# Kernel optimization log

Hardware: AMD Instinct MI355X
Metric: run time of the kernel (lower is better)

The kernel has to match this reference:

```python
import jax, jax.numpy as jnp
import numpy as np

B, V, NB, NJ, NEXTRA = 512, 6890, 10, 24, 9
PARENTS = np.array([-1,0,0,0,1,2,3,4,5,6,7,8,9,9,9,12,13,14,16,17,18,19,20,21], dtype=np.int32)


def setup_inputs() -> dict:
    key = jax.random.key(0)
    ks = jax.random.split(key, 11)
    betas = jax.random.normal(ks[0], (B, NB + 1), jnp.float32) * 0.1
    betas = betas.at[:, 0].set(1.0)  # col 0 is a global scale in this SMPL variant
    body_pose = jax.random.normal(ks[1], (B, 3 * (NJ - 1)), jnp.float32) * 0.2
    global_orient = jax.random.normal(ks[2], (B, 3), jnp.float32) * 0.2
    transl = jax.random.normal(ks[3], (B, 3), jnp.float32) * 0.1
    model_scale_opt = jnp.ones((1,), jnp.float32)
    smpl_v_template = jax.random.normal(ks[4], (V, 3), jnp.float32)
    smil_v_template = jax.random.normal(ks[5], (V, 3), jnp.float32)
    shapedirs = jax.random.normal(ks[6], (V, 3, NB), jnp.float32) * 0.01
    J_regressor = jax.nn.softmax(jax.random.normal(ks[7], (NJ, V), jnp.float32), axis=1)
    lbs_weights = jax.nn.softmax(jax.random.normal(ks[8], (V, NJ), jnp.float32) * 4.0, axis=1)
    J_regressor_extra = jax.nn.softmax(jax.random.normal(ks[9], (NEXTRA, V), jnp.float32), axis=1)
    parents = jnp.asarray(PARENTS)
    return dict(betas=betas, body_pose=body_pose, global_orient=global_orient,
                transl=transl, model_scale_opt=model_scale_opt,
                smpl_v_template=smpl_v_template, smil_v_template=smil_v_template,
                shapedirs=shapedirs, J_regressor=J_regressor, lbs_weights=lbs_weights,
                J_regressor_extra=J_regressor_extra, parents=parents)


def batch_rodrigues(rvecs):
    # rvecs: [N,3] axis-angle -> [N,3,3] rotation matrices
    angle = jnp.linalg.norm(rvecs + 1e-8, axis=1, keepdims=True)  # [N,1]
    axis = rvecs / angle
    c = jnp.cos(angle)[..., None]  # [N,1,1]
    s = jnp.sin(angle)[..., None]
    rx, ry, rz = axis[:, 0], axis[:, 1], axis[:, 2]
    z = jnp.zeros_like(rx)
    K = jnp.stack([z, -rz, ry, rz, z, -rx, -ry, rx, z], axis=1).reshape(-1, 3, 3)
    I = jnp.eye(3, dtype=rvecs.dtype)
    return I + s * K + (1.0 - c) * jnp.matmul(K, K)


def _smpl_forward(betas, body_pose, global_orient, transl, model_scale_opt,
                  smpl_v_template, smil_v_template, shapedirs,
                  J_regressor, lbs_weights, J_regressor_extra):
    dtype = betas.dtype
    # ---- updateShape ----
    s = model_scale_opt[0]
    v_template = smpl_v_template * s + (1.0 - s) * smil_v_template  # [V,3]
    blend_shape = jnp.einsum('bl,mkl->bmk', betas[:, 1:], shapedirs)  # [B,V,3]
    v_shaped = (v_template[None] + blend_shape) * betas[:, :1, None]  # scale col
    J_shaped = jnp.einsum('bik,ji->bjk', v_shaped, J_regressor)  # [B,NJ,3]

    # ---- updatePose ----
    full_pose = jnp.concatenate([global_orient, body_pose], axis=1)  # [B,NJ*3]
    rot_mats = batch_rodrigues(full_pose.reshape(-1, 3)).reshape(B, NJ, 3, 3)

    # relative joint locations w.r.t. parents
    rel_joints = J_shaped.at[:, 1:].add(-J_shaped[:, PARENTS[1:]])
    top = jnp.concatenate([rot_mats, rel_joints[..., None]], axis=-1)  # [B,NJ,3,4]
    bottom = jnp.broadcast_to(
        jnp.array([0.0, 0.0, 0.0, 1.0], dtype=dtype), (B, NJ, 1, 4))
    mats = jnp.concatenate([top, bottom], axis=2)  # [B,NJ,4,4]

    # sequential kinematic-chain composition over the 24-joint tree
    chain = [mats[:, 0]]
    for i in range(1, NJ):
        chain.append(jnp.matmul(chain[PARENTS[i]], mats[:, i]))
    chain = jnp.stack(chain, axis=1)  # [B,NJ,4,4]
    posed_joints = chain[:, :, :3, 3]  # [B,NJ,3]

    # relative transforms: subtract rotated rest joints
    corr = jnp.einsum('bjmn,bjn->bjm', chain[:, :, :3, :3], J_shaped)
    A = chain.at[:, :, :3, 3].add(-corr)  # [B,NJ,4,4]

    # linear blend skinning
    T = jnp.einsum('vj,bjmn->bvmn', lbs_weights, A)  # [B,V,4,4]
    verts = jnp.einsum('bvmn,bvn->bvm', T[:, :, :3, :3], v_shaped) + T[:, :, :3, 3]

    extra_joints = jnp.einsum('bik,ji->bjk', verts, J_regressor_extra)  # [B,9,3]
    joints = jnp.concatenate([posed_joints, extra_joints], axis=1)  # [B,33,3]

    t = transl[:, None, :]
    # concat verts and joints along point dim for a single output array
    return jnp.concatenate([verts + t, joints + t], axis=1)  # [B, V+33, 3]


def reference(betas, body_pose, global_orient, transl, model_scale_opt,
              smpl_v_template, smil_v_template, shapedirs,
              J_regressor, lbs_weights, J_regressor_extra, parents):
    return _smpl_forward(betas, body_pose, global_orient, transl, model_scale_opt,
                         smpl_v_template, smil_v_template, shapedirs,
                         J_regressor, lbs_weights, J_regressor_extra)
```

## Files before the change

kernel.cpp:

```cpp
#include <hip/hip_runtime.h>


#define BATCH 512
#define NV 6890
#define NBD 10
#define NJ 24
#define NEXTRA 9
#define NOUT (NV + NJ + NEXTRA)
#define VBLK ((NV + 255) / 256)
#define BPB 4
#define ECHUNK ((NV + 3) / 4)
#define PCHUNK 8
#define PCLEN ((NV + PCHUNK - 1) / PCHUNK)

__constant__ int c_par[NJ] = {-1,0,0,0,1,2,3,4,5,6,7,8,9,9,9,12,13,14,16,17,18,19,20,21};
__constant__ int c_dep[NJ] = {0,1,1,1,2,2,2,3,3,3,4,4,4,4,4,5,5,5,6,6,7,7,8,8};

__global__ __launch_bounds__(256) void precompute_kernel(
    const float* __restrict__ jreg,
    const float* __restrict__ smpl_t,
    const float* __restrict__ smil_t,
    const float* __restrict__ sdirs,
    const float* __restrict__ msc,
    float* __restrict__ jtjs_part)
{
    const int c = blockIdx.x;
    const int j = blockIdx.y;
    const float s = msc[0];

    const int vbeg = c * PCLEN;
    const int vend_ = (vbeg + PCLEN < NV) ? vbeg + PCLEN : NV;

    float acc[33];
#pragma unroll
    for (int i = 0; i < 33; ++i) acc[i] = 0.f;

    for (int v = vbeg + threadIdx.x; v < vend_; v += 256) {
        const float w = jreg[j * NV + v];
#pragma unroll
        for (int k = 0; k < 3; ++k) {
            float vt = s * smpl_t[v * 3 + k] + (1.f - s) * smil_t[v * 3 + k];
            acc[k] = fmaf(w, vt, acc[k]);
        }
        const float2* sd2 = (const float2*)(sdirs + (size_t)v * 30);
#pragma unroll
        for (int i = 0; i < 15; ++i) {
            float2 x = sd2[i];
            acc[3 + 2 * i]     = fmaf(w, x.x, acc[3 + 2 * i]);
            acc[3 + 2 * i + 1] = fmaf(w, x.y, acc[3 + 2 * i + 1]);
        }
    }

#pragma unroll
    for (int i = 0; i < 33; ++i) {
        float x = acc[i];
        for (int off = 32; off; off >>= 1) x += __shfl_xor(x, off, 64);
        acc[i] = x;
    }

    __shared__ float red[4][33];
    const int lane = threadIdx.x & 63, wv = threadIdx.x >> 6;
    if (lane == 0) {
#pragma unroll
        for (int i = 0; i < 33; ++i) red[wv][i] = acc[i];
    }
    __syncthreads();
    if (threadIdx.x < 33) {
        jtjs_part[(c * NJ + j) * 33 + threadIdx.x] =
            red[0][threadIdx.x] + red[1][threadIdx.x]
          + red[2][threadIdx.x] + red[3][threadIdx.x];
    }
}

__global__ __launch_bounds__(64) void joints_kernel(
    const float* __restrict__ betas,
    const float* __restrict__ body_pose,
    const float* __restrict__ glob_or,
    const float* __restrict__ transl,
    const float* __restrict__ jtjs_part,
    float* __restrict__ wsA,
    float* __restrict__ out)
{
    const int b = blockIdx.x;
    const int j = threadIdx.x;

    __shared__ float sJ[NJ][3];
    __shared__ float mats[NJ][12];
    __shared__ float chain[NJ][12];
    __shared__ float sbeta[NBD + 1];

    if (threadIdx.x < NBD + 1) sbeta[threadIdx.x] = betas[b * (NBD + 1) + threadIdx.x];

    if (threadIdx.x >= NJ && threadIdx.x < NJ + 3 * NEXTRA)
        out[((size_t)b * NOUT + NV + NJ) * 3 + (threadIdx.x - NJ)] = 0.f;

    __syncthreads();

    if (j < NJ) {
        float jt[33];
#pragma unroll
        for (int i = 0; i < 33; ++i) jt[i] = 0.f;
        for (int c = 0; c < PCHUNK; ++c) {
#pragma unroll
            for (int i = 0; i < 33; ++i) jt[i] += jtjs_part[(c * NJ + j) * 33 + i];
        }

        const float beta0 = sbeta[0];
#pragma unroll
        for (int k = 0; k < 3; ++k) {
            float a = jt[k];
#pragma unroll
            for (int l = 0; l < NBD; ++l) a = fmaf(sbeta[1 + l], jt[3 + k * 10 + l], a);
            sJ[j][k] = a * beta0;
        }
        float rx, ry, rz;
        if (j == 0) {
            rx = glob_or[b * 3 + 0]; ry = glob_or[b * 3 + 1]; rz = glob_or[b * 3 + 2];
        } else {
            rx = body_pose[b * 69 + (j - 1) * 3 + 0];
            ry = body_pose[b * 69 + (j - 1) * 3 + 1];
            rz = body_pose[b * 69 + (j - 1) * 3 + 2];
        }
        float ex = rx + 1e-8f, ey = ry + 1e-8f, ez = rz + 1e-8f;
        float ang = sqrtf(ex * ex + ey * ey + ez * ez);
        float inv = 1.f / ang;
        float ax = rx * inv, ay = ry * inv, az = rz * inv;
        float c = cosf(ang), s = sinf(ang), t = 1.f - c;
        mats[j][0]  = 1.f + t * (-(ay * ay + az * az));
        mats[j][1]  = -s * az + t * (ax * ay);
        mats[j][2]  =  s * ay + t * (ax * az);
        mats[j][4]  =  s * az + t * (ax * ay);
        mats[j][5]  = 1.f + t * (-(ax * ax + az * az));
        mats[j][6]  = -s * ax + t * (ay * az);
        mats[j][8]  = -s * ay + t * (ax * az);
        mats[j][9]  =  s * ax + t * (ay * az);
        mats[j][10] = 1.f + t * (-(ax * ax + ay * ay));
    }
    __syncthreads();
    if (j < NJ) {
        const int p = c_par[j];
        float t0 = sJ[j][0], t1 = sJ[j][1], t2 = sJ[j][2];
        if (p >= 0) { t0 -= sJ[p][0]; t1 -= sJ[p][1]; t2 -= sJ[p][2]; }
        mats[j][3] = t0; mats[j][7] = t1; mats[j][11] = t2;
    }
    __syncthreads();
    if (j == 0) {
#pragma unroll
        for (int k = 0; k < 12; ++k) chain[0][k] = mats[0][k];
    }
    __syncthreads();
    for (int lev = 1; lev <= 8; ++lev) {
        if (j < NJ && c_dep[j] == lev) {
            const int p = c_par[j];
            float r_[12];
#pragma unroll
            for (int r = 0; r < 3; ++r) {
#pragma unroll
                for (int col = 0; col < 4; ++col) {
                    float acc = (col == 3) ? chain[p][r * 4 + 3] : 0.f;
#pragma unroll
                    for (int q = 0; q < 3; ++q) acc = fmaf(chain[p][r * 4 + q], mats[j][q * 4 + col], acc);
                    r_[r * 4 + col] = acc;
                }
            }
#pragma unroll
            for (int k = 0; k < 12; ++k) chain[j][k] = r_[k];
        }
        __syncthreads();
    }
    if (j < NJ) {
        float A[12];
#pragma unroll
        for (int k = 0; k < 12; ++k) A[k] = chain[j][k];
        const float c0 = A[3], c1 = A[7], c2 = A[11];
        const float j0 = sJ[j][0], j1 = sJ[j][1], j2 = sJ[j][2];
        A[3]  = c0 - (A[0] * j0 + A[1] * j1 + A[2]  * j2);
        A[7]  = c1 - (A[4] * j0 + A[5] * j1 + A[6]  * j2);
        A[11] = c2 - (A[8] * j0 + A[9] * j1 + A[10] * j2);
#pragma unroll
        for (int k = 0; k < 12; ++k) wsA[((size_t)b * NJ + j) * 12 + k] = A[k];
        const float tx = transl[b * 3 + 0], ty = transl[b * 3 + 1], tz = transl[b * 3 + 2];
        const size_t o = ((size_t)b * NOUT + NV + j) * 3;
        out[o + 0] = c0 + tx; out[o + 1] = c1 + ty; out[o + 2] = c2 + tz;
    }
}

__global__ __launch_bounds__(256) void lbs_kernel(
    const float* __restrict__ betas,
    const float* __restrict__ transl,
    const float* __restrict__ msc,
    const float* __restrict__ smpl_t,
    const float* __restrict__ smil_t,
    const float* __restrict__ sdirs,
    const float* __restrict__ lbsw,
    const float* __restrict__ wsA,
    float* __restrict__ out)
{
    const int v = blockIdx.x * 256 + threadIdx.x;
    const bool valid = v < NV;
    const int vc = valid ? v : NV - 1;
    const int b0 = blockIdx.y * BPB;
    const float s = msc[0];

    float vt[3];
#pragma unroll
    for (int k = 0; k < 3; ++k)
        vt[k] = s * smpl_t[vc * 3 + k] + (1.f - s) * smil_t[vc * 3 + k];

    float sd[30];
    {
        const float2* sd2 = (const float2*)(sdirs + (size_t)vc * 30);
#pragma unroll
        for (int i = 0; i < 15; ++i) { float2 x = sd2[i]; sd[2 * i] = x.x; sd[2 * i + 1] = x.y; }
    }
    float w[NJ];
    {
        const float4* w4 = (const float4*)(lbsw + (size_t)vc * NJ);
#pragma unroll
        for (int i = 0; i < 6; ++i) {
            float4 x = w4[i];
            w[4 * i] = x.x; w[4 * i + 1] = x.y; w[4 * i + 2] = x.z; w[4 * i + 3] = x.w;
        }
    }

#pragma unroll
    for (int bb = 0; bb < BPB; ++bb) {
        const int b = b0 + bb;
        const float* __restrict__ Bb = betas + b * (NBD + 1);
        const float* __restrict__ Ab = wsA + (size_t)b * NJ * 12;

        float vs[3];
#pragma unroll
        for (int k = 0; k < 3; ++k) {
            float a = vt[k];
#pragma unroll
            for (int l = 0; l < NBD; ++l) a = fmaf(Bb[1 + l], sd[k * 10 + l], a);
            vs[k] = a * Bb[0];
        }

        float T[12];
#pragma unroll
        for (int k = 0; k < 12; ++k) T[k] = 0.f;
#pragma unroll 4
        for (int jj = 0; jj < NJ; ++jj) {
            const float ww = w[jj];
#pragma unroll
            for (int k = 0; k < 12; ++k) T[k] = fmaf(ww, Ab[jj * 12 + k], T[k]);
        }

        if (valid) {
            const float tx = transl[b * 3 + 0], ty = transl[b * 3 + 1], tz = transl[b * 3 + 2];
            const size_t o = ((size_t)b * NOUT + v) * 3;
            out[o + 0] = fmaf(T[0], vs[0], fmaf(T[1], vs[1], fmaf(T[2],  vs[2], T[3])))  + tx;
            out[o + 1] = fmaf(T[4], vs[0], fmaf(T[5], vs[1], fmaf(T[6],  vs[2], T[7])))  + ty;
            out[o + 2] = fmaf(T[8], vs[0], fmaf(T[9], vs[1], fmaf(T[10], vs[2], T[11]))) + tz;
        }
    }
}

__global__ __launch_bounds__(256) void extra_kernel(
    const float* __restrict__ jre,
    float* out)
{
    const int b = blockIdx.y;
    const int v0 = blockIdx.x * ECHUNK;
    int vend = v0 + ECHUNK; if (vend > NV) vend = NV;
    const float* vb = out + (size_t)b * NOUT * 3;

    float acc[27];
#pragma unroll
    for (int i = 0; i < 27; ++i) acc[i] = 0.f;

    for (int v = v0 + threadIdx.x; v < vend; v += 256) {
        const float x = vb[v * 3 + 0], y = vb[v * 3 + 1], z = vb[v * 3 + 2];
#pragma unroll
        for (int e = 0; e < NEXTRA; ++e) {
            const float we = jre[e * NV + v];
            acc[e * 3 + 0] = fmaf(we, x, acc[e * 3 + 0]);
            acc[e * 3 + 1] = fmaf(we, y, acc[e * 3 + 1]);
            acc[e * 3 + 2] = fmaf(we, z, acc[e * 3 + 2]);
        }
    }

#pragma unroll
    for (int i = 0; i < 27; ++i) {
        float x = acc[i];
        for (int off = 32; off; off >>= 1) x += __shfl_xor(x, off, 64);
        acc[i] = x;
    }
    __shared__ float red[4][27];
    const int lane = threadIdx.x & 63, wv = threadIdx.x >> 6;
    if (lane == 0) {
#pragma unroll
        for (int i = 0; i < 27; ++i) red[wv][i] = acc[i];
    }
    __syncthreads();
    if (threadIdx.x < 27) {
        const float sum = red[0][threadIdx.x] + red[1][threadIdx.x]
                        + red[2][threadIdx.x] + red[3][threadIdx.x];
        atomicAdd(&out[((size_t)b * NOUT + NV + NJ) * 3 + threadIdx.x], sum);
    }
}

extern "C" void kernel_launch(void* const* d_in, const int* in_sizes, int n_in,
                              void* d_out, int out_size, void* d_ws, size_t ws_size,
                              hipStream_t stream) {
    const float* betas     = (const float*)d_in[0];
    const float* body_pose = (const float*)d_in[1];
    const float* glob_or   = (const float*)d_in[2];
    const float* transl    = (const float*)d_in[3];
    const float* msc       = (const float*)d_in[4];
    const float* smpl_t    = (const float*)d_in[5];
    const float* smil_t    = (const float*)d_in[6];
    const float* sdirs     = (const float*)d_in[7];
    const float* jreg      = (const float*)d_in[8];
    const float* lbsw      = (const float*)d_in[9];
    const float* jre       = (const float*)d_in[10];

    float* out  = (float*)d_out;
    float* ws   = (float*)d_ws;
    float* wsA       = ws;
    float* jtjs_part = ws + (size_t)BATCH * NJ * 12;

    dim3 gA(PCHUNK, NJ);
    precompute_kernel<<<gA, 256, 0, stream>>>(jreg, smpl_t, smil_t, sdirs, msc, jtjs_part);

    joints_kernel<<<BATCH, 64, 0, stream>>>(betas, body_pose, glob_or, transl, jtjs_part, wsA, out);

    dim3 gC(VBLK, BATCH / BPB);
    lbs_kernel<<<gC, 256, 0, stream>>>(betas, transl, msc, smpl_t, smil_t, sdirs, lbsw, wsA, out);

    dim3 gE(4, BATCH);
    extra_kernel<<<gE, 256, 0, stream>>>(jre, out);
}
```

Measured before the change: 175.3 us.

## Compute extra joints algebraically from joint transforms instead of re-reading posed vertices

Because extra joints are linear in the per-joint transforms, the change precomputes, for each extra joint and body joint, the regressor-times-skinning-weight contractions of the template and shape directions, which do not depend on the batch. The joints kernel then forms the extra joints from these precomputed sums, the betas and the 24 transforms. This removes the extra_kernel pass, which re-read all posed vertices for every batch element and used atomics. The cost is extra blocks in the precompute kernel, and the floating-point summation order changes.

```diff
diff --git a/kernel.cpp b/kernel.cpp
--- a/kernel.cpp
+++ b/kernel.cpp
@@ -9,66 +9,111 @@
 #define NOUT (NV + NJ + NEXTRA)
 #define VBLK ((NV + 255) / 256)
 #define BPB 4
-#define ECHUNK ((NV + 3) / 4)
 #define PCHUNK 8
 #define PCLEN ((NV + PCHUNK - 1) / PCHUNK)
+#define EPN 34
 
 __constant__ int c_par[NJ] = {-1,0,0,0,1,2,3,4,5,6,7,8,9,9,9,12,13,14,16,17,18,19,20,21};
 __constant__ int c_dep[NJ] = {0,1,1,1,2,2,2,3,3,3,4,4,4,4,4,5,5,5,6,6,7,7,8,8};
 
-__global__ __launch_bounds__(256) void precompute_kernel(
+__global__ __launch_bounds__(256) void pre_kernel(
     const float* __restrict__ jreg,
+    const float* __restrict__ jre,
+    const float* __restrict__ lbsw,
     const float* __restrict__ smpl_t,
     const float* __restrict__ smil_t,
     const float* __restrict__ sdirs,
     const float* __restrict__ msc,
-    float* __restrict__ jtjs_part)
+    float* __restrict__ jtjs_part,
+    float* __restrict__ epre)
 {
-    const int c = blockIdx.x;
     const int j = blockIdx.y;
     const float s = msc[0];
 
-    const int vbeg = c * PCLEN;
-    const int vend_ = (vbeg + PCLEN < NV) ? vbeg + PCLEN : NV;
-
-    float acc[33];
-#pragma unroll
-    for (int i = 0; i < 33; ++i) acc[i] = 0.f;
-
-    for (int v = vbeg + threadIdx.x; v < vend_; v += 256) {
-        const float w = jreg[j * NV + v];
-#pragma unroll
-        for (int k = 0; k < 3; ++k) {
-            float vt = s * smpl_t[v * 3 + k] + (1.f - s) * smil_t[v * 3 + k];
-            acc[k] = fmaf(w, vt, acc[k]);
-        }
-        const float2* sd2 = (const float2*)(sdirs + (size_t)v * 30);
-#pragma unroll
-        for (int i = 0; i < 15; ++i) {
-            float2 x = sd2[i];
-            acc[3 + 2 * i]     = fmaf(w, x.x, acc[3 + 2 * i]);
-            acc[3 + 2 * i + 1] = fmaf(w, x.y, acc[3 + 2 * i + 1]);
-        }
-    }
-
-#pragma unroll
-    for (int i = 0; i < 33; ++i) {
-        float x = acc[i];
-        for (int off = 32; off; off >>= 1) x += __shfl_xor(x, off, 64);
-        acc[i] = x;
-    }
-
-    __shared__ float red[4][33];
+    __shared__ float red[4][EPN];
     const int lane = threadIdx.x & 63, wv = threadIdx.x >> 6;
-    if (lane == 0) {
-#pragma unroll
-        for (int i = 0; i < 33; ++i) red[wv][i] = acc[i];
-    }
-    __syncthreads();
-    if (threadIdx.x < 33) {
-        jtjs_part[(c * NJ + j) * 33 + threadIdx.x] =
-            red[0][threadIdx.x] + red[1][threadIdx.x]
-          + red[2][threadIdx.x] + red[3][threadIdx.x];
+
+    if (blockIdx.x < PCHUNK) {
+        const int c = blockIdx.x;
+        const int vbeg = c * PCLEN;
+        const int vend_ = (vbeg + PCLEN < NV) ? vbeg + PCLEN : NV;
+
+        float acc[33];
+#pragma unroll
+        for (int i = 0; i < 33; ++i) acc[i] = 0.f;
+
+        for (int v = vbeg + threadIdx.x; v < vend_; v += 256) {
+            const float w = jreg[j * NV + v];
+#pragma unroll
+            for (int k = 0; k < 3; ++k) {
+                float vt = s * smpl_t[v * 3 + k] + (1.f - s) * smil_t[v * 3 + k];
+                acc[k] = fmaf(w, vt, acc[k]);
+            }
+            const float2* sd2 = (const float2*)(sdirs + (size_t)v * 30);
+#pragma unroll
+            for (int i = 0; i < 15; ++i) {
+                float2 x = sd2[i];
+                acc[3 + 2 * i]     = fmaf(w, x.x, acc[3 + 2 * i]);
+                acc[3 + 2 * i + 1] = fmaf(w, x.y, acc[3 + 2 * i + 1]);
+            }
+        }
+
+#pragma unroll
+        for (int i = 0; i < 33; ++i) {
+            float x = acc[i];
+            for (int off = 32; off; off >>= 1) x += __shfl_xor(x, off, 64);
+            acc[i] = x;
+        }
+        if (lane == 0) {
+#pragma unroll
+            for (int i = 0; i < 33; ++i) red[wv][i] = acc[i];
+        }
+        __syncthreads();
+        if (threadIdx.x < 33) {
+            jtjs_part[(c * NJ + j) * 33 + threadIdx.x] =
+                red[0][threadIdx.x] + red[1][threadIdx.x]
+              + red[2][threadIdx.x] + red[3][threadIdx.x];
+        }
+    } else {
+        const int e = blockIdx.x - PCHUNK;
+
+        float acc[EPN];
+#pragma unroll
+        for (int i = 0; i < EPN; ++i) acc[i] = 0.f;
+
+        for (int v = threadIdx.x; v < NV; v += 256) {
+            const float u = jre[e * NV + v] * lbsw[(size_t)v * NJ + j];
+            acc[33] += u;
+#pragma unroll
+            for (int k = 0; k < 3; ++k) {
+                float vt = s * smpl_t[v * 3 + k] + (1.f - s) * smil_t[v * 3 + k];
+                acc[k] = fmaf(u, vt, acc[k]);
+            }
+            const float2* sd2 = (const float2*)(sdirs + (size_t)v * 30);
+#pragma unroll
+            for (int i = 0; i < 15; ++i) {
+                float2 x = sd2[i];
+                acc[3 + 2 * i]     = fmaf(u, x.x, acc[3 + 2 * i]);
+                acc[3 + 2 * i + 1] = fmaf(u, x.y, acc[3 + 2 * i + 1]);
+            }
+        }
+
+#pragma unroll
+        for (int i = 0; i < EPN; ++i) {
+            float x = acc[i];
+            for (int off = 32; off; off >>= 1) x += __shfl_xor(x, off, 64);
+            acc[i] = x;
+        }
+        if (lane == 0) {
+#pragma unroll
+            for (int i = 0; i < EPN; ++i) red[wv][i] = acc[i];
+        }
+        __syncthreads();
+        if (threadIdx.x < EPN) {
+            epre[(e * NJ + j) * EPN + threadIdx.x] =
+                red[0][threadIdx.x] + red[1][threadIdx.x]
+              + red[2][threadIdx.x] + red[3][threadIdx.x];
+        }
     }
 }
 
@@ -78,6 +123,7 @@
     const float* __restrict__ glob_or,
     const float* __restrict__ transl,
     const float* __restrict__ jtjs_part,
+    const float* __restrict__ epre,
     float* __restrict__ wsA,
     float* __restrict__ out)
 {
@@ -88,12 +134,10 @@
     __shared__ float mats[NJ][12];
     __shared__ float chain[NJ][12];
     __shared__ float sbeta[NBD + 1];
+    __shared__ float sS[NEXTRA][NJ][3];
+    __shared__ float sW[NEXTRA][NJ];
 
     if (threadIdx.x < NBD + 1) sbeta[threadIdx.x] = betas[b * (NBD + 1) + threadIdx.x];
-
-    if (threadIdx.x >= NJ && threadIdx.x < NJ + 3 * NEXTRA)
-        out[((size_t)b * NOUT + NV + NJ) * 3 + (threadIdx.x - NJ)] = 0.f;
-
     __syncthreads();
 
     if (j < NJ) {
@@ -179,9 +223,42 @@
         A[11] = c2 - (A[8] * j0 + A[9] * j1 + A[10] * j2);
 #pragma unroll
         for (int k = 0; k < 12; ++k) wsA[((size_t)b * NJ + j) * 12 + k] = A[k];
+#pragma unroll
+        for (int k = 0; k < 12; ++k) mats[j][k] = A[k];
         const float tx = transl[b * 3 + 0], ty = transl[b * 3 + 1], tz = transl[b * 3 + 2];
         const size_t o = ((size_t)b * NOUT + NV + j) * 3;
         out[o + 0] = c0 + tx; out[o + 1] = c1 + ty; out[o + 2] = c2 + tz;
+    }
+
+    for (int idx = threadIdx.x; idx < NEXTRA * NJ * 3; idx += 64) {
+        const int e  = idx / (NJ * 3);
+        const int r  = idx - e * NJ * 3;
+        const int jj = r / 3;
+        const int cc = r - jj * 3;
+        const float* ep = epre + (e * NJ + jj) * EPN;
+        float a = ep[cc];
+#pragma unroll
+        for (int l = 0; l < NBD; ++l) a = fmaf(sbeta[1 + l], ep[3 + cc * 10 + l], a);
+        sS[e][jj][cc] = a * sbeta[0];
+    }
+    for (int idx = threadIdx.x; idx < NEXTRA * NJ; idx += 64) {
+        const int e  = idx / NJ;
+        const int jj = idx - e * NJ;
+        sW[e][jj] = epre[(e * NJ + jj) * EPN + 33];
+    }
+    __syncthreads();
+    if (threadIdx.x < 3 * NEXTRA) {
+        const int e = threadIdx.x / 3;
+        const int k = threadIdx.x - e * 3;
+        float acc = 0.f;
+#pragma unroll 4
+        for (int jj = 0; jj < NJ; ++jj) {
+            acc = fmaf(mats[jj][k * 4 + 0], sS[e][jj][0], acc);
+            acc = fmaf(mats[jj][k * 4 + 1], sS[e][jj][1], acc);
+            acc = fmaf(mats[jj][k * 4 + 2], sS[e][jj][2], acc);
+            acc = fmaf(mats[jj][k * 4 + 3], sW[e][jj],    acc);
+        }
+        out[((size_t)b * NOUT + NV + NJ) * 3 + threadIdx.x] = acc + transl[b * 3 + k];
     }
 }
 
@@ -258,50 +335,6 @@
     }
 }
 
-__global__ __launch_bounds__(256) void extra_kernel(
-    const float* __restrict__ jre,
-    float* out)
-{
-    const int b = blockIdx.y;
-    const int v0 = blockIdx.x * ECHUNK;
-    int vend = v0 + ECHUNK; if (vend > NV) vend = NV;
-    const float* vb = out + (size_t)b * NOUT * 3;
-
-    float acc[27];
-#pragma unroll
-    for (int i = 0; i < 27; ++i) acc[i] = 0.f;
-
-    for (int v = v0 + threadIdx.x; v < vend; v += 256) {
-        const float x = vb[v * 3 + 0], y = vb[v * 3 + 1], z = vb[v * 3 + 2];
-#pragma unroll
-        for (int e = 0; e < NEXTRA; ++e) {
-            const float we = jre[e * NV + v];
-            acc[e * 3 + 0] = fmaf(we, x, acc[e * 3 + 0]);
-            acc[e * 3 + 1] = fmaf(we, y, acc[e * 3 + 1]);
-            acc[e * 3 + 2] = fmaf(we, z, acc[e * 3 + 2]);
-        }
-    }
-
-#pragma unroll
-    for (int i = 0; i < 27; ++i) {
-        float x = acc[i];
-        for (int off = 32; off; off >>= 1) x += __shfl_xor(x, off, 64);
-        acc[i] = x;
-    }
-    __shared__ float red[4][27];
-    const int lane = threadIdx.x & 63, wv = threadIdx.x >> 6;
-    if (lane == 0) {
-#pragma unroll
-        for (int i = 0; i < 27; ++i) red[wv][i] = acc[i];
-    }
-    __syncthreads();
-    if (threadIdx.x < 27) {
-        const float sum = red[0][threadIdx.x] + red[1][threadIdx.x]
-                        + red[2][threadIdx.x] + red[3][threadIdx.x];
-        atomicAdd(&out[((size_t)b * NOUT + NV + NJ) * 3 + threadIdx.x], sum);
-    }
-}
-
 extern "C" void kernel_launch(void* const* d_in, const int* in_sizes, int n_in,
                               void* d_out, int out_size, void* d_ws, size_t ws_size,
                               hipStream_t stream) {
@@ -320,16 +353,16 @@
     float* out  = (float*)d_out;
     float* ws   = (float*)d_ws;
     float* wsA       = ws;
-    float* jtjs_part = ws + (size_t)BATCH * NJ * 12;
-
-    dim3 gA(PCHUNK, NJ);
-    precompute_kernel<<<gA, 256, 0, stream>>>(jreg, smpl_t, smil_t, sdirs, msc, jtjs_part);
-
-    joints_kernel<<<BATCH, 64, 0, stream>>>(betas, body_pose, glob_or, transl, jtjs_part, wsA, out);
+    float* jtjs_part = wsA + (size_t)BATCH * NJ * 12;
+    float* epre      = jtjs_part + PCHUNK * NJ * 33;
+
+    dim3 gA(PCHUNK + NEXTRA, NJ);
+    pre_kernel<<<gA, 256, 0, stream>>>(jreg, jre, lbsw, smpl_t, smil_t, sdirs, msc,
+                                       jtjs_part, epre);
+
+    joints_kernel<<<BATCH, 64, 0, stream>>>(betas, body_pose, glob_or, transl,
+                                            jtjs_part, epre, wsA, out);
 
     dim3 gC(VBLK, BATCH / BPB);
     lbs_kernel<<<gC, 256, 0, stream>>>(betas, transl, msc, smpl_t, smil_t, sdirs, lbsw, wsA, out);
-
-    dim3 gE(4, BATCH);
-    extra_kernel<<<gE, 256, 0, stream>>>(jre, out);
 }
```

New measurement: 193.9 us. 10.6% more time.
